# Kernel optimization log

Hardware: AMD Instinct MI355X
Metric: run time of the kernel (lower is better)

Reference implementation:

```python
import jax, jax.numpy as jnp
import numpy as np
from functools import partial

TAU_MEM = 10.0
TAU_SYN = (5.0, 10.0)
THRESHOLD = 1.0
WINDOW = 0.3
BATCH = 32
T = 256
N_SYN = 2
N_NEURONS = 2048


@jax.custom_vjp
def spike_fn(v_shifted):
    # Heaviside of (vmem - threshold); surrogate gradient is a boxcar of width `window`.
    return (v_shifted > 0).astype(v_shifted.dtype)


def _spike_fwd(v_shifted):
    return spike_fn(v_shifted), v_shifted


def _spike_bwd(v_shifted, g):
    surr = (jnp.abs(v_shifted) < WINDOW).astype(g.dtype) / WINDOW
    return (g * surr,)


spike_fn.defvjp(_spike_fwd, _spike_bwd)


def setup_inputs() -> dict:
    key = jax.random.key(0)
    # Poisson-like analog spike input, shape (batch*T, n_syn, n_neurons)
    binary_input = (jax.random.uniform(key, (BATCH * T, N_SYN, N_NEURONS), dtype=jnp.float32) < 0.1
                    ).astype(jnp.float32)
    return {"binary_input": binary_input}


def reference(binary_input):
    # (B*T, n_syn, N) -> (B, T, n_syn, N) -> time-major, synapse-last: (T, B, N, n_syn)
    x = binary_input.reshape(BATCH, T, N_SYN, N_NEURONS).transpose(1, 0, 3, 2)

    alpha_mem = jnp.exp(jnp.float32(-1.0 / TAU_MEM))
    alpha_syn = jnp.exp(-1.0 / jnp.asarray(TAU_SYN, dtype=jnp.float32))  # [n_syn]

    def step(carry, inp_t):
        vmem, isyn = carry                      # vmem [B,N], isyn [B,N,n_syn]
        isyn = alpha_syn * isyn + inp_t         # leaky synaptic integration
        vmem = alpha_mem * vmem + isyn.sum(-1)  # leaky membrane integration
        spikes = spike_fn(vmem - THRESHOLD)     # threshold crossing
        vmem = vmem - spikes * THRESHOLD        # reset by subtraction
        return (vmem, isyn), spikes

    v0 = jnp.zeros((BATCH, N_NEURONS), dtype=x.dtype)
    i0 = jnp.zeros((BATCH, N_NEURONS, N_SYN), dtype=x.dtype)
    _, all_spikes = jax.lax.scan(step, (v0, i0), x)  # [T, B, N]

    # back to (batch*T, N) as in the torch module's trailing reshape
    return all_spikes.transpose(1, 0, 2).reshape(-1, N_NEURONS)
```

## Files before the change

### kernel.cpp

```cpp
#include <hip/hip_runtime.h>
#include <math.h>

#define T_STEPS 256
#define N_NEUR  2048
#define N_BATCH 32
#define STRIDE  (2 * N_NEUR)

#define TT      16
#define NTILE   (T_STEPS / TT)
#define BN      64

__device__ __forceinline__ void async_cp16(const float* g, float* l) {
    __builtin_amdgcn_global_load_lds(
        (const __attribute__((address_space(1))) void*)g,
        (__attribute__((address_space(3))) void*)l,
        16, 0, 0);
}

__global__ __launch_bounds__(64) void snn_scan_kernel(
    const float* __restrict__ in,
    float* __restrict__ out,
    float a_mem, float a_s0, float a_s1)
{
    __shared__ float buf[2][TT * 2 * BN];

    const int tid = threadIdx.x;
    const int bid = blockIdx.x;
    const int b   = bid >> 5;
    const int n0  = (bid & 31) << 6;

    const float* gin = in + (size_t)b * T_STEPS * STRIDE + n0;
    float* pout      = out + (size_t)b * T_STEPS * N_NEUR + n0 + tid;

    const int p_lo  = tid >> 4;
    const int lane4 = (tid & 15) * 4;
    const int ldsf = tid * 4;

    #pragma unroll
    for (int j = 0; j < 8; ++j) {
        const int p = 4 * j + p_lo;
        const float* g = gin + (size_t)(p >> 1) * STRIDE + (p & 1) * N_NEUR + lane4;
        async_cp16(g, &buf[0][j * 256 + ldsf]);
    }
    __syncthreads();

    float vmem = 0.0f, i0 = 0.0f, i1 = 0.0f;

    #pragma unroll
    for (int k = 0; k < NTILE; ++k) {
        if (k + 1 < NTILE) {
            const float* gt = gin + (size_t)(k + 1) * TT * STRIDE;
            float* lb = &buf[(k + 1) & 1][0];
            #pragma unroll
            for (int j = 0; j < 8; ++j) {
                const int p = 4 * j + p_lo;
                const float* g = gt + (size_t)(p >> 1) * STRIDE + (p & 1) * N_NEUR + lane4;
                async_cp16(g, lb + j * 256 + ldsf);
            }
        }

        const float* lb = &buf[k & 1][0];
        float* po = pout + (size_t)k * TT * N_NEUR;

        #pragma unroll
        for (int t = 0; t < TT; ++t) {
            const float x0 = lb[t * 128 + tid];
            const float x1 = lb[t * 128 + BN + tid];

            i0 = __fadd_rn(__fmul_rn(a_s0, i0), x0);
            i1 = __fadd_rn(__fmul_rn(a_s1, i1), x1);

            const float ssum = __fadd_rn(i0, i1);
            vmem = __fadd_rn(__fmul_rn(a_mem, vmem), ssum);

            const float vs = __fsub_rn(vmem, 1.0f);
            const bool fired = (vs > 0.0f);
            po[(size_t)t * N_NEUR] = fired ? 1.0f : 0.0f;
            vmem = fired ? vs : vmem;
        }
        __syncthreads();
    }
}

extern "C" void kernel_launch(void* const* d_in, const int* in_sizes, int n_in,
                              void* d_out, int out_size, void* d_ws, size_t ws_size,
                              hipStream_t stream) {
    const float* in = (const float*)d_in[0];
    float* out = (float*)d_out;

    const float a_s0  = (float)exp((double)(-1.0f / 5.0f));
    const float a_s1  = (float)exp((double)(-1.0f / 10.0f));
    const float a_mem = (float)exp((double)(-1.0f / 10.0f));

    dim3 block(64);
    dim3 grid(N_BATCH * (N_NEUR / BN));

    snn_scan_kernel<<<grid, block, 0, stream>>>(in, out, a_mem, a_s0, a_s1);
}
```

Before: 217.7 us.

## Triple-buffer input tiles with explicit vmcnt waits and batched spike stores

Moves from double to triple buffering of the LDS input tiles, so two tiles of global-to-LDS loads are in flight ahead of compute. The per-tile __syncthreads is replaced by hand-counted s_waitcnt vmcnt values; this is safe only because each block is a single 64-lane wave. The 16 spike outputs per tile are now kept in registers and stored after the tile's compute instead of inside the recurrence loop. The goal is to hide global memory latency in a low-occupancy, latency-bound scan. The cost is more LDS per block and wait counts that must stay correct, since they include the outstanding stores.

Measured after the change: 216.8 us. About the same (-0.4%).

```diff
diff --git a/kernel.cpp b/kernel.cpp
--- a/kernel.cpp
+++ b/kernel.cpp
@@ -9,20 +9,22 @@
 #define TT      16
 #define NTILE   (T_STEPS / TT)
 #define BN      64
+#define NBUF    3
 
 __device__ __forceinline__ void async_cp16(const float* g, float* l) {
     __builtin_amdgcn_global_load_lds(
         (const __attribute__((address_space(1))) void*)g,
-        (__attribute__((address_space(3))) void*)l,
-        16, 0, 0);
+        (__attribute__((address_space(3))) void*)l, 16, 0, 0);
 }
+
+#define WAIT_VMCNT(n) asm volatile("s_waitcnt vmcnt(" #n ")" ::: "memory")
 
 __global__ __launch_bounds__(64) void snn_scan_kernel(
     const float* __restrict__ in,
     float* __restrict__ out,
     float a_mem, float a_s0, float a_s1)
 {
-    __shared__ float buf[2][TT * 2 * BN];
+    __shared__ float buf[NBUF][TT * 2 * BN];
 
     const int tid = threadIdx.x;
     const int bid = blockIdx.x;
@@ -34,33 +36,35 @@
 
     const int p_lo  = tid >> 4;
     const int lane4 = (tid & 15) * 4;
-    const int ldsf = tid * 4;
+    const int ldsf  = tid * 4;
 
-    #pragma unroll
-    for (int j = 0; j < 8; ++j) {
-        const int p = 4 * j + p_lo;
-        const float* g = gin + (size_t)(p >> 1) * STRIDE + (p & 1) * N_NEUR + lane4;
-        async_cp16(g, &buf[0][j * 256 + ldsf]);
-    }
-    __syncthreads();
+    auto issue = [&](int k) {
+        const float* gt = gin + (size_t)k * TT * STRIDE;
+        float* lb = &buf[k % NBUF][0];
+        #pragma unroll
+        for (int j = 0; j < 8; ++j) {
+            const int p = 4 * j + p_lo;
+            async_cp16(gt + (size_t)(p >> 1) * STRIDE + (p & 1) * N_NEUR + lane4,
+                       lb + j * 256 + ldsf);
+        }
+    };
+
+    issue(0);
+    issue(1);
 
     float vmem = 0.0f, i0 = 0.0f, i1 = 0.0f;
 
     #pragma unroll
     for (int k = 0; k < NTILE; ++k) {
-        if (k + 1 < NTILE) {
-            const float* gt = gin + (size_t)(k + 1) * TT * STRIDE;
-            float* lb = &buf[(k + 1) & 1][0];
-            #pragma unroll
-            for (int j = 0; j < 8; ++j) {
-                const int p = 4 * j + p_lo;
-                const float* g = gt + (size_t)(p >> 1) * STRIDE + (p & 1) * N_NEUR + lane4;
-                async_cp16(g, lb + j * 256 + ldsf);
-            }
-        }
+        if (k + 2 < NTILE) issue(k + 2);
 
-        const float* lb = &buf[k & 1][0];
-        float* po = pout + (size_t)k * TT * N_NEUR;
+        if      (k == 0)         WAIT_VMCNT(16);
+        else if (k == 1)         WAIT_VMCNT(32);
+        else if (k == NTILE - 1) WAIT_VMCNT(32);
+        else                     WAIT_VMCNT(40);
+
+        const float* lb = &buf[k % NBUF][0];
+        float sp[TT];
 
         #pragma unroll
         for (int t = 0; t < TT; ++t) {
@@ -75,10 +79,15 @@
 
             const float vs = __fsub_rn(vmem, 1.0f);
             const bool fired = (vs > 0.0f);
-            po[(size_t)t * N_NEUR] = fired ? 1.0f : 0.0f;
+            sp[t] = fired ? 1.0f : 0.0f;
             vmem = fired ? vs : vmem;
         }
-        __syncthreads();
+
+        float* po = pout + (size_t)k * TT * N_NEUR;
+        #pragma unroll
+        for (int t = 0; t < TT; ++t) {
+            po[(size_t)t * N_NEUR] = sp[t];
+        }
     }
 }
 
```
